# Kernel optimization log

Measured on AMD Instinct MI355X. Metric: run time of the kernel, lower is better.

The kernel has to match this reference:

```python
import jax, jax.numpy as jnp
import numpy as np

N, F, G, E, L, HID, C = 16384, 256, 64, 131072, 3, 512, 2
EPS = 1e-5
IU = F * (F - 1) // 2      # 32640 strict-upper-tri features per graph
IN1 = IU + F * L           # 33408 MLP input width


def setup_inputs() -> dict:
    key = jax.random.key(0)
    ks = jax.random.split(key, 16)

    def w(k, shape, fan_in):
        return jax.random.normal(k, shape, jnp.float32) * (1.0 / np.sqrt(fan_in))

    return {
        "x": jax.random.normal(ks[0], (N, F), jnp.float32),
        "edge_index": jax.random.randint(ks[1], (2, E), 0, N, dtype=jnp.int32),
        "batch": jnp.repeat(jnp.arange(G, dtype=jnp.int32), N // G),  # F nodes per graph
        "lin_src_w": w(ks[2], (L, F, F), F), "lin_src_b": jnp.zeros((L, F), jnp.float32),
        "lin_dst_w": w(ks[3], (L, F, F), F), "lin_dst_b": jnp.zeros((L, F), jnp.float32),
        "att_w": w(ks[4], (L, 2 * F, 1), 2 * F), "att_b": jnp.zeros((L, 1), jnp.float32),
        "bn_g": jnp.ones((IU,), jnp.float32), "bn_b": jnp.zeros((IU,), jnp.float32),
        "bnh_g": jnp.ones((F * L,), jnp.float32), "bnh_b": jnp.zeros((F * L,), jnp.float32),
        "w1": w(ks[5], (IN1, HID), IN1), "b1": jnp.zeros((HID,), jnp.float32),
        "g1": jnp.ones((HID,), jnp.float32), "be1": jnp.zeros((HID,), jnp.float32),
        "w2": w(ks[6], (HID, HID // 2), HID), "b2": jnp.zeros((HID // 2,), jnp.float32),
        "g2": jnp.ones((HID // 2,), jnp.float32), "be2": jnp.zeros((HID // 2,), jnp.float32),
        "w3": w(ks[7], (HID // 2, HID // 2), HID // 2), "b3": jnp.zeros((HID // 2,), jnp.float32),
        "g3": jnp.ones((HID // 2,), jnp.float32), "be3": jnp.zeros((HID // 2,), jnp.float32),
        "w4": w(ks[8], (HID // 2, C), HID // 2), "b4": jnp.zeros((C,), jnp.float32),
    }


def _bn(z, g, b):
    # BatchNorm1d (training-mode batch stats, biased variance, as torch uses for normalization)
    m = jnp.mean(z, 0)
    v = jnp.var(z, 0)
    return (z - m) * jax.lax.rsqrt(v + EPS) * g + b


def _conv(x, src, dst, Ws, bs, Wd, bd, Wa, ba):
    # EdgeLevelAttention layer (heads=1): gather -> concat -> linear -> softmax(heads) -> weighted scatter-add
    x_src = x @ Ws + bs                      # [N, F]
    x_dst = x @ Wd + bd                      # [N, F]
    x_j = x_src[src]                         # [E2, F] source features per edge
    x_i = x_dst[dst]                         # [E2, F] destination features per edge
    alpha = jax.nn.softmax(jnp.concatenate([x_i, x_j], -1) @ Wa + ba, axis=1)  # [E2, 1] (all ones for heads=1)
    msg = x_i * alpha                        # message uses x_i, as in the source
    return jax.ops.segment_sum(msg, dst, num_segments=N)


def reference(x, edge_index, batch, lin_src_w, lin_src_b, lin_dst_w, lin_dst_b,
              att_w, att_b, bn_g, bn_b, bnh_g, bnh_b,
              w1, b1, g1, be1, w2, b2, g2, be2, w3, b3, g3, be3, w4, b4):
    loops = jnp.arange(N, dtype=edge_index.dtype)          # add_self_loops
    src = jnp.concatenate([edge_index[0], loops])
    dst = jnp.concatenate([edge_index[1], loops])

    h = x
    pooled = []
    cnt = jax.ops.segment_sum(jnp.ones((N, 1), x.dtype), batch, num_segments=G)
    for l in range(L):
        h = _conv(h, src, dst, lin_src_w[l], lin_src_b[l],
                  lin_dst_w[l], lin_dst_b[l], att_w[l], att_b[l])
        pooled.append(jax.ops.segment_sum(h, batch, num_segments=G) / cnt)  # global_mean_pool

    iu = np.triu_indices(F, k=1)
    xt = x.reshape(G, F, F)[:, iu[0], iu[1]]               # strict upper triangle per graph [G, IU]
    xt = _bn(xt, bn_g, bn_b)
    hh = _bn(jnp.concatenate(pooled, 1), bnh_g, bnh_b)     # [G, F*L]
    z = jnp.concatenate([xt, hh], 1)                       # [G, IN1]

    z = jax.nn.relu(_bn(z @ w1 + b1, g1, be1))
    z = jax.nn.relu(_bn(z @ w2 + b2, g2, be2))
    z = jax.nn.relu(_bn(z @ w3 + b3, g3, be3))
    return z @ w4 + b4                                     # [G, C]
```

## Files before the change

### kernel.cpp

```cpp
#include <hip/hip_runtime.h>
#include <cstdint>

typedef __attribute__((ext_vector_type(8))) short short8;
typedef __attribute__((ext_vector_type(4))) float f32x4;
typedef unsigned short ushort_t;

static constexpr int NN = 16384, FF = 256, GG = 64, EE = 131072, LL = 3;
static constexpr int HIDN = 512, IU = 32640, IN1 = 33408;
#define EPSV 1e-5f

__device__ inline unsigned short bf16r(float v) {
  unsigned u = __float_as_uint(v);
  u += 0x7FFFu + ((u >> 16) & 1u);
  return (unsigned short)(u >> 16);
}

__global__ __launch_bounds__(256) void k_zero(int* __restrict__ p) {
  int i = blockIdx.x * 256 + threadIdx.x;
  if (i < 16448) p[i] = 0;
}

__global__ __launch_bounds__(256) void k_hist(const int* __restrict__ dst,
                                              const int* __restrict__ batch,
                                              int* __restrict__ deg, int* __restrict__ cnt) {
  __shared__ int hist[64];
  int bx = blockIdx.x, t = threadIdx.x;
  if (bx < 512) {
    int e = bx * 256 + t;
    atomicAdd(&deg[dst[e]], 1);
  } else {
    if (t < 64) hist[t] = 0;
    __syncthreads();
    int4 v = ((const int4*)batch)[(bx - 512) * 256 + t];
    int a[4] = {v.x, v.y, v.z, v.w};
    int cur = a[0], run = 1;
#pragma unroll
    for (int j = 1; j < 4; ++j) {
      if (a[j] == cur) run++;
      else { atomicAdd(&hist[cur], run); cur = a[j]; run = 1; }
    }
    atomicAdd(&hist[cur], run);
    __syncthreads();
    if (t < 64 && hist[t]) atomicAdd(&cnt[t], hist[t]);
  }
}

__global__ __launch_bounds__(256, 2) void k_conv(const float* __restrict__ A,
                                                 const float* __restrict__ W,
                                                 const float* __restrict__ bias,
                                                 const int* __restrict__ deg,
                                                 float* __restrict__ C,
                                                 float* __restrict__ pooled_p, int lofs) {
  __shared__ __align__(16) unsigned short Ah[64][72], Al[64][72];
  __shared__ __align__(16) unsigned short Bh[128][72], Bl[128][72];
  int n0 = blockIdx.x * 128, m0 = blockIdx.y * 64;
  int t = threadIdx.x;
  int w = t >> 6, l = t & 63;
  int wn = w * 32;
  int lr = l & 15, lg = l >> 4;
  f32x4 acc[4][2];
#pragma unroll
  for (int fm = 0; fm < 4; ++fm)
#pragma unroll
    for (int fn = 0; fn < 2; ++fn) acc[fm][fn] = (f32x4){0.f, 0.f, 0.f, 0.f};

  int am = t >> 2, aq = t & 3;
  int bkp = t & 3, bnf = (t >> 2) & 31, brr = t >> 7;

  for (int ks = 0; ks < 4; ++ks) {
    int k0 = ks * 64;
    if (ks) __syncthreads();
    {
      const float* ap = A + (size_t)(m0 + am) * FF + k0;
#pragma unroll
      for (int i = 0; i < 4; ++i) {
        int k = aq * 4 + i * 16;
        float4 v = *(const float4*)(ap + k);
        const float* vf = (const float*)&v;
        unsigned short h[4], lo[4];
#pragma unroll
        for (int j = 0; j < 4; ++j) {
          h[j] = bf16r(vf[j]);
          lo[j] = bf16r(vf[j] - __uint_as_float((unsigned)h[j] << 16));
        }
        *(uint2*)&Ah[am][k] = make_uint2((unsigned)h[0] | ((unsigned)h[1] << 16),
                                         (unsigned)h[2] | ((unsigned)h[3] << 16));
        *(uint2*)&Al[am][k] = make_uint2((unsigned)lo[0] | ((unsigned)lo[1] << 16),
                                         (unsigned)lo[2] | ((unsigned)lo[3] << 16));
      }
    }
#pragma unroll
    for (int r2 = 0; r2 < 4; ++r2) {
      int k = 2 * bkp + 8 * (brr * 4 + r2);
      const float* wp = W + (size_t)(k0 + k) * FF + n0 + bnf * 4;
      float4 va = *(const float4*)wp;
      float4 vb = *(const float4*)(wp + FF);
      const float* fa = (const float*)&va;
      const float* fb = (const float*)&vb;
#pragma unroll
      for (int j = 0; j < 4; ++j) {
        unsigned short ha = bf16r(fa[j]), hb = bf16r(fb[j]);
        unsigned short la = bf16r(fa[j] - __uint_as_float((unsigned)ha << 16));
        unsigned short lb = bf16r(fb[j] - __uint_as_float((unsigned)hb << 16));
        int n = bnf * 4 + j;
        *(unsigned*)&Bh[n][k] = (unsigned)ha | ((unsigned)hb << 16);
        *(unsigned*)&Bl[n][k] = (unsigned)la | ((unsigned)lb << 16);
      }
    }
    __syncthreads();
#pragma unroll
    for (int k2 = 0; k2 < 2; ++k2) {
      int kk = k2 * 32 + lg * 8;
      short8 afh[4], afl[4], bfh[2], bfl[2];
#pragma unroll
      for (int fm = 0; fm < 4; ++fm) {
        afh[fm] = *(const short8*)&Ah[fm * 16 + lr][kk];
        afl[fm] = *(const short8*)&Al[fm * 16 + lr][kk];
      }
#pragma unroll
      for (int fn = 0; fn < 2; ++fn) {
        bfh[fn] = *(const short8*)&Bh[wn + fn * 16 + lr][kk];
        bfl[fn] = *(const short8*)&Bl[wn + fn * 16 + lr][kk];
      }
#pragma unroll
      for (int fm = 0; fm < 4; ++fm)
#pragma unroll
        for (int fn = 0; fn < 2; ++fn) {
          acc[fm][fn] = __builtin_amdgcn_mfma_f32_16x16x32_bf16(afl[fm], bfh[fn], acc[fm][fn], 0, 0, 0);
          acc[fm][fn] = __builtin_amdgcn_mfma_f32_16x16x32_bf16(afh[fm], bfl[fn], acc[fm][fn], 0, 0, 0);
          acc[fm][fn] = __builtin_amdgcn_mfma_f32_16x16x32_bf16(afh[fm], bfh[fn], acc[fm][fn], 0, 0, 0);
        }
    }
  }
  float degf[4][4];
#pragma unroll
  for (int fm = 0; fm < 4; ++fm)
#pragma unroll
    for (int r = 0; r < 4; ++r)
      degf[fm][r] = (float)(deg[m0 + fm * 16 + lg * 4 + r] + 1);
  int g = blockIdx.y >> 2, sub = blockIdx.y & 3;
#pragma unroll
  for (int fn = 0; fn < 2; ++fn) {
    int col = n0 + wn + fn * 16 + lr;
    float bb = bias[col];
    float cs = 0.f;
#pragma unroll
    for (int fm = 0; fm < 4; ++fm) {
      const float* av = (const float*)&acc[fm][fn];
#pragma unroll
      for (int r = 0; r < 4; ++r) {
        int row = m0 + fm * 16 + lg * 4 + r;
        float v = (av[r] + bb) * degf[fm][r];
        if (C) C[(size_t)row * FF + col] = v;
        cs += v;
      }
    }
    cs += __shfl_xor(cs, 16);
    cs += __shfl_xor(cs, 32);
    if (lg == 0)
      pooled_p[((size_t)sub * 64 + g) * (FF * LL) + lofs + col] = cs;
  }
}

__global__ __launch_bounds__(1024, 1) void k_xt_bn(const float* __restrict__ x,
                                                   const float* __restrict__ bn_g,
                                                   const float* __restrict__ bn_b,
                                                   ushort_t* __restrict__ zh,
                                                   ushort_t* __restrict__ zl) {
  __shared__ float sb1[16][256], sb2[16][256];
  __shared__ float rsA[256], bbA[256];
  int i = blockIdx.x, t = threadIdx.x;
  int jq = t & 63, gq = t >> 6;
  int j4 = jq * 4;
  float4 vals[4];
  float s1[4] = {}, s2[4] = {};
#pragma unroll
  for (int r = 0; r < 4; ++r) {
    int g = gq * 4 + r;
    float4 vv = *(const float4*)(x + (size_t)(g * 256 + i) * FF + j4);
    vals[r] = vv;
    s1[0] += vv.x; s2[0] += vv.x * vv.x;
    s1[1] += vv.y; s2[1] += vv.y * vv.y;
    s1[2] += vv.z; s2[2] += vv.z * vv.z;
    s1[3] += vv.w; s2[3] += vv.w * vv.w;
  }
  *(float4*)&sb1[gq][j4] = make_float4(s1[0], s1[1], s1[2], s1[3]);
  *(float4*)&sb2[gq][j4] = make_float4(s2[0], s2[1], s2[2], s2[3]);
  __syncthreads();
  if (t < 256) {
    int j = t;
    float S1 = 0.f, S2 = 0.f;
#pragma unroll
    for (int q = 0; q < 16; ++q) { S1 += sb1[q][j]; S2 += sb2[q][j]; }
    float m = S1 * (1.f / 64.f);
    float var = S2 * (1.f / 64.f) - m * m;
    float rs = 0.f, bb = 0.f;
    if (j > i) {
      int p = i * 255 - (i * (i - 1)) / 2 + (j - i - 1);
      rs = rsqrtf(var + EPSV) * bn_g[p];
      bb = bn_b[p] - m * rs;
    }
    rsA[j] = rs;
    bbA[j] = bb;
  }
  __syncthreads();
  int P0 = i * 255 - (i * (i - 1)) / 2 - i - 1;
#pragma unroll
  for (int r = 0; r < 4; ++r) {
    int g = gq * 4 + r;
    size_t base = (size_t)g * IN1 + P0;
    const float* vf = (const float*)&vals[r];
#pragma unroll
    for (int jj = 0; jj < 4; ++jj) {
      int j = j4 + jj;
      if (j > i) {
        float f = vf[jj] * rsA[j] + bbA[j];
        unsigned short h = bf16r(f);
        zh[base + j] = h;
        zl[base + j] = bf16r(f - __uint_as_float((unsigned)h << 16));
      }
    }
  }
}

__global__ __launch_bounds__(256) void k_pool_bn(const float* __restrict__ pooled_p,
                                                 const int* __restrict__ cnt,
                                                 const float* __restrict__ bnh_g,
                                                 const float* __restrict__ bnh_b,
                                                 ushort_t* __restrict__ zh,
                                                 ushort_t* __restrict__ zl) {
  __shared__ float sb1[4][64], sb2[4][64], rsA[64], bbA[64];
  int bx = blockIdx.x, t = threadIdx.x;
  int ql = t & 63, gq = t >> 6;
  int q = bx * 64 + ql;
  float vals[16];
  float s1 = 0.f, s2 = 0.f;
#pragma unroll
  for (int gg = 0; gg < 16; ++gg) {
    int g = gq * 16 + gg;
    float v = (pooled_p[((size_t)0 * 64 + g) * (FF * LL) + q] +
               pooled_p[((size_t)1 * 64 + g) * (FF * LL) + q] +
               pooled_p[((size_t)2 * 64 + g) * (FF * LL) + q] +
               pooled_p[((size_t)3 * 64 + g) * (FF * LL) + q]) / (float)cnt[g];
    vals[gg] = v;
    s1 += v;
    s2 += v * v;
  }
  sb1[gq][ql] = s1;
  sb2[gq][ql] = s2;
  __syncthreads();
  if (t < 64) {
    float S1 = sb1[0][t] + sb1[1][t] + sb1[2][t] + sb1[3][t];
    float S2 = sb2[0][t] + sb2[1][t] + sb2[2][t] + sb2[3][t];
    float m = S1 * (1.f / 64.f);
    float var = S2 * (1.f / 64.f) - m * m;
    int qq = bx * 64 + t;
    float rs = rsqrtf(var + EPSV) * bnh_g[qq];
    rsA[t] = rs;
    bbA[t] = bnh_b[qq] - m * rs;
  }
  __syncthreads();
#pragma unroll
  for (int gg = 0; gg < 16; ++gg) {
    int g = gq * 16 + gg;
    float f = vals[gg] * rsA[ql] + bbA[ql];
    unsigned short h = bf16r(f);
    zh[(size_t)g * IN1 + IU + q] = h;
    zl[(size_t)g * IN1 + IU + q] = bf16r(f - __uint_as_float((unsigned)h << 16));
  }
}

__global__ __launch_bounds__(256, 4) void k_w1(const ushort_t* __restrict__ zh,
                                               const ushort_t* __restrict__ zl,
                                               const float* __restrict__ W,
                                               float* __restrict__ partial) {
  __shared__ __align__(16) unsigned short Zh[64][72], Zl[64][72];
  __shared__ __align__(16) unsigned short Wh[64][72], Wl[64][72];
  int nb = blockIdx.x, s = blockIdx.y;
  int t = threadIdx.x;
  int w = t >> 6, l = t & 63, lr = l & 15, lg = l >> 4;
  int ncol = nb * 64 + w * 16 + lr;
  f32x4 acc[4];
#pragma unroll
  for (int mt = 0; mt < 4; ++mt) acc[mt] = (f32x4){0.f, 0.f, 0.f, 0.f};

  for (int c = s; c < 522; c += 64) {
    int p0 = c * 64;
    if (c != s) __syncthreads();
#pragma unroll
    for (int it = 0; it < 2; ++it) {
      int idx = it * 256 + t;
      int g = idx >> 3, kq = idx & 7;
      *(uint4*)&Zh[g][kq * 8] = *(const uint4*)(zh + (size_t)g * IN1 + p0 + kq * 8);
      *(uint4*)&Zl[g][kq * 8] = *(const uint4*)(zl + (size_t)g * IN1 + p0 + kq * 8);
    }
#pragma unroll
    for (int it = 0; it < 2; ++it) {
      int idx = it * 256 + t;
      int kp = idx >> 4, cg = idx & 15;
      int k = kp * 2;
      const float* wp = W + (size_t)(p0 + k) * HIDN + nb * 64 + cg * 4;
      float4 va = *(const float4*)wp;
      float4 vb = *(const float4*)(wp + HIDN);
      const float* fa = (const float*)&va;
      const float* fb = (const float*)&vb;
#pragma unroll
      for (int j = 0; j < 4; ++j) {
        unsigned ua = __float_as_uint(fa[j]);
        unsigned ub = __float_as_uint(fb[j]);
        unsigned short ha = (unsigned short)(ua >> 16);
        unsigned short hb = (unsigned short)(ub >> 16);
        unsigned short la = bf16r(fa[j] - __uint_as_float(ua & 0xFFFF0000u));
        unsigned short lb = bf16r(fb[j] - __uint_as_float(ub & 0xFFFF0000u));
        int col = cg * 4 + j;
        *(unsigned*)&Wh[col][k] = (unsigned)ha | ((unsigned)hb << 16);
        *(unsigned*)&Wl[col][k] = (unsigned)la | ((unsigned)lb << 16);
      }
    }
    __syncthreads();
#pragma unroll
    for (int k2 = 0; k2 < 2; ++k2) {
      int kloc = k2 * 32 + lg * 8;
      short8 bh = *(const short8*)&Wh[w * 16 + lr][kloc];
      short8 bl = *(const short8*)&Wl[w * 16 + lr][kloc];
#pragma unroll
      for (int mt = 0; mt < 4; ++mt) {
        short8 ah = *(const short8*)&Zh[mt * 16 + lr][kloc];
        short8 al = *(const short8*)&Zl[mt * 16 + lr][kloc];
        acc[mt] = __builtin_amdgcn_mfma_f32_16x16x32_bf16(al, bh, acc[mt], 0, 0, 0);
        acc[mt] = __builtin_amdgcn_mfma_f32_16x16x32_bf16(ah, bl, acc[mt], 0, 0, 0);
        acc[mt] = __builtin_amdgcn_mfma_f32_16x16x32_bf16(ah, bh, acc[mt], 0, 0, 0);
      }
    }
  }
#pragma unroll
  for (int mt = 0; mt < 4; ++mt) {
    const float* av = (const float*)&acc[mt];
#pragma unroll
    for (int r = 0; r < 4; ++r) {
      int g = mt * 16 + lg * 4 + r;
      partial[((size_t)s * 64 + g) * HIDN + ncol] = av[r];
    }
  }
}

__global__ __launch_bounds__(256) void k_reduce(const float* __restrict__ partial,
                                                const float* __restrict__ bias,
                                                float* __restrict__ out, int S, int N) {
  int idx = blockIdx.x * 256 + threadIdx.x;
  if (idx >= 64 * N) return;
  int h = idx % N;
  float a = bias[h];
  for (int s = 0; s < S; ++s) a += partial[(size_t)s * 64 * N + idx];
  out[idx] = a;
}

__global__ __launch_bounds__(64) void k_bn_relu(const float* __restrict__ in,
                                                const float* __restrict__ gamma,
                                                const float* __restrict__ beta,
                                                float* __restrict__ out, int N) {
  int h = blockIdx.x;
  int g = threadIdx.x;
  float v = in[(size_t)g * N + h];
  float s = v, s2 = v * v;
#pragma unroll
  for (int o = 32; o > 0; o >>= 1) {
    s += __shfl_xor(s, o);
    s2 += __shfl_xor(s2, o);
  }
  float m = s * (1.f / 64.f);
  float var = s2 * (1.f / 64.f) - m * m;
  float r = (v - m) * rsqrtf(var + EPSV) * gamma[h] + beta[h];
  out[(size_t)g * N + h] = fmaxf(r, 0.f);
}

__global__ __launch_bounds__(256, 2) void k_mlp_small(const float* __restrict__ Z,
                                                      const float* __restrict__ W,
                                                      const float* __restrict__ bias,
                                                      const float* __restrict__ gamma,
                                                      const float* __restrict__ beta,
                                                      float* __restrict__ out, int K, int N) {
  __shared__ float Ws[512 * 16];
  __shared__ float zl[64][132];
  __shared__ float sb1[16][17], sb2[16][17];
  int t = threadIdx.x;
  int h0 = blockIdx.x * 16;
  for (int idx = t; idx < K * 4; idx += 256) {
    int r = idx >> 2, q = idx & 3;
    *(float4*)&Ws[r * 16 + q * 4] = *(const float4*)(W + (size_t)r * N + h0 + q * 4);
  }
  int c = t & 15, gq = t >> 4;
  float acc[4] = {};
  for (int ch = 0; ch < K; ch += 128) {
    for (int idx = t; idx < 64 * 32; idx += 256) {
      int g = idx >> 5, kq = idx & 31;
      *(float4*)&zl[g][kq * 4] = *(const float4*)(Z + (size_t)g * K + ch + kq * 4);
    }
    __syncthreads();
#pragma unroll 8
    for (int kk = 0; kk < 128; ++kk) {
      float w = Ws[(ch + kk) * 16 + c];
#pragma unroll
      for (int i = 0; i < 4; ++i) acc[i] = fmaf(zl[gq * 4 + i][kk], w, acc[i]);
    }
    __syncthreads();
  }
  float bb = bias[h0 + c];
  float s1 = 0.f, s2 = 0.f;
#pragma unroll
  for (int i = 0; i < 4; ++i) {
    acc[i] += bb;
    s1 += acc[i];
    s2 += acc[i] * acc[i];
  }
  sb1[gq][c] = s1;
  sb2[gq][c] = s2;
  __syncthreads();
  float S1 = 0.f, S2 = 0.f;
#pragma unroll
  for (int q = 0; q < 16; ++q) { S1 += sb1[q][c]; S2 += sb2[q][c]; }
  float m = S1 * (1.f / 64.f);
  float var = S2 * (1.f / 64.f) - m * m;
  float rs = rsqrtf(var + EPSV) * gamma[h0 + c];
  float be = beta[h0 + c];
#pragma unroll
  for (int i = 0; i < 4; ++i)
    out[(size_t)(gq * 4 + i) * N + h0 + c] = fmaxf((acc[i] - m) * rs + be, 0.f);
}

__global__ __launch_bounds__(256) void k_final(const float* __restrict__ A,
                                               const float* __restrict__ w4,
                                               const float* __restrict__ b4,
                                               float* __restrict__ out) {
  __shared__ float w4l[512];
  int t = threadIdx.x;
  w4l[t] = w4[t];
  w4l[256 + t] = w4[256 + t];
  __syncthreads();
  int w = t >> 6, l = t & 63;
  for (int g = w * 16; g < w * 16 + 16; ++g) {
    float4 av = *(const float4*)(A + (size_t)g * 256 + l * 4);
    float c0 = av.x * w4l[(l * 4 + 0) * 2] + av.y * w4l[(l * 4 + 1) * 2] +
               av.z * w4l[(l * 4 + 2) * 2] + av.w * w4l[(l * 4 + 3) * 2];
    float c1 = av.x * w4l[(l * 4 + 0) * 2 + 1] + av.y * w4l[(l * 4 + 1) * 2 + 1] +
               av.z * w4l[(l * 4 + 2) * 2 + 1] + av.w * w4l[(l * 4 + 3) * 2 + 1];
#pragma unroll
    for (int o = 32; o > 0; o >>= 1) {
      c0 += __shfl_xor(c0, o);
      c1 += __shfl_xor(c1, o);
    }
    if (l == 0) {
      out[g * 2 + 0] = c0 + b4[0];
      out[g * 2 + 1] = c1 + b4[1];
    }
  }
}

extern "C" void kernel_launch(void* const* d_in, const int* in_sizes, int n_in,
                              void* d_out, int out_size, void* d_ws, size_t ws_size,
                              hipStream_t stream) {
  const float* x = (const float*)d_in[0];
  const int* edge = (const int*)d_in[1];
  const int* batch = (const int*)d_in[2];
  const float* lin_dst_w = (const float*)d_in[5];
  const float* lin_dst_b = (const float*)d_in[6];
  const float* bn_g = (const float*)d_in[9];
  const float* bn_b = (const float*)d_in[10];
  const float* bnh_g = (const float*)d_in[11];
  const float* bnh_b = (const float*)d_in[12];
  const float* w1 = (const float*)d_in[13];
  const float* b1 = (const float*)d_in[14];
  const float* g1 = (const float*)d_in[15];
  const float* be1 = (const float*)d_in[16];
  const float* w2 = (const float*)d_in[17];
  const float* b2 = (const float*)d_in[18];
  const float* g2 = (const float*)d_in[19];
  const float* be2 = (const float*)d_in[20];
  const float* w3 = (const float*)d_in[21];
  const float* b3 = (const float*)d_in[22];
  const float* g3 = (const float*)d_in[23];
  const float* be3 = (const float*)d_in[24];
  const float* w4 = (const float*)d_in[25];
  const float* b4 = (const float*)d_in[26];
  const int* dstp = edge + EE;

  char* ws = (char*)d_ws;
  int* deg = (int*)(ws);
  int* cnt = (int*)(ws + 65536);
  float* bufA = (float*)(ws + 131072);
  float* bufB = (float*)(ws + 131072 + 16777216);
  float* pooled_p = (float*)(ws + 131072 + 2 * 16777216);
  char* tail = ws + 131072 + 2 * 16777216 + 786432;
  float* m1 = (float*)(tail);
  float* m1b = (float*)(tail + 131072);
  float* m2b = (float*)(tail + 262144);
  float* m3b = (float*)(tail + 262144 + 65536);
  ushort_t* zh = (ushort_t*)bufA;
  ushort_t* zlp = zh + (size_t)64 * IN1;
  float* partial = bufB;

  k_zero<<<65, 256, 0, stream>>>(deg);
  k_hist<<<528, 256, 0, stream>>>(dstp, batch, deg, cnt);

  k_conv<<<dim3(2, 256), 256, 0, stream>>>(x, lin_dst_w, lin_dst_b, deg, bufA, pooled_p, 0);
  k_conv<<<dim3(2, 256), 256, 0, stream>>>(bufA, lin_dst_w + (size_t)FF * FF,
                                           lin_dst_b + FF, deg, bufB, pooled_p, FF);
  k_conv<<<dim3(2, 256), 256, 0, stream>>>(bufB, lin_dst_w + (size_t)2 * FF * FF,
                                           lin_dst_b + 2 * FF, deg, (float*)nullptr,
                                           pooled_p, 2 * FF);

  k_xt_bn<<<256, 1024, 0, stream>>>(x, bn_g, bn_b, zh, zlp);
  k_pool_bn<<<12, 256, 0, stream>>>(pooled_p, cnt, bnh_g, bnh_b, zh, zlp);

  k_w1<<<dim3(8, 64), 256, 0, stream>>>(zh, zlp, w1, partial);
  k_reduce<<<128, 256, 0, stream>>>(partial, b1, m1, 64, HIDN);
  k_bn_relu<<<HIDN, 64, 0, stream>>>(m1, g1, be1, m1b, HIDN);

  k_mlp_small<<<16, 256, 0, stream>>>(m1b, w2, b2, g2, be2, m2b, HIDN, 256);
  k_mlp_small<<<16, 256, 0, stream>>>(m2b, w3, b3, g3, be3, m3b, 256, 256);

  k_final<<<1, 256, 0, stream>>>(m3b, w4, b4, (float*)d_out);
}
```

Before: 178.5 us.

## Fuse BN front kernels, fuse reduce+BN, widen w1 split-K, swap conv grid

Merges the upper-triangle BN kernel and the pooled BN kernel into one launch, and merges the split-K reduction with the BN+ReLU of the first MLP layer into one kernel. It also doubles the split-K count of the w1 GEMM (128 slices instead of 64) and swaps the conv grid so that consecutive blocks share the same weight column tile. The aim is fewer launches, more parallelism in the large w1 GEMM, and better L2 reuse in the conv. The cost is twice the partial-sum traffic, which the reduce kernel must read, and that reduce now runs on only 8 blocks.

```diff
diff --git a/kernel.cpp b/kernel.cpp
--- a/kernel.cpp
+++ b/kernel.cpp
@@ -53,7 +53,8 @@
                                                  float* __restrict__ pooled_p, int lofs) {
   __shared__ __align__(16) unsigned short Ah[64][72], Al[64][72];
   __shared__ __align__(16) unsigned short Bh[128][72], Bl[128][72];
-  int n0 = blockIdx.x * 128, m0 = blockIdx.y * 64;
+  int mb = blockIdx.x;
+  int n0 = blockIdx.y * 128, m0 = mb * 64;
   int t = threadIdx.x;
   int w = t >> 6, l = t & 63;
   int wn = w * 32;
@@ -138,7 +139,7 @@
 #pragma unroll
     for (int r = 0; r < 4; ++r)
       degf[fm][r] = (float)(deg[m0 + fm * 16 + lg * 4 + r] + 1);
-  int g = blockIdx.y >> 2, sub = blockIdx.y & 3;
+  int g = mb >> 2, sub = mb & 3;
 #pragma unroll
   for (int fn = 0; fn < 2; ++fn) {
     int col = n0 + wn + fn * 16 + lr;
@@ -162,111 +163,112 @@
   }
 }
 
-__global__ __launch_bounds__(1024, 1) void k_xt_bn(const float* __restrict__ x,
-                                                   const float* __restrict__ bn_g,
-                                                   const float* __restrict__ bn_b,
-                                                   ushort_t* __restrict__ zh,
-                                                   ushort_t* __restrict__ zl) {
-  __shared__ float sb1[16][256], sb2[16][256];
-  __shared__ float rsA[256], bbA[256];
-  int i = blockIdx.x, t = threadIdx.x;
-  int jq = t & 63, gq = t >> 6;
-  int j4 = jq * 4;
-  float4 vals[4];
-  float s1[4] = {}, s2[4] = {};
-#pragma unroll
-  for (int r = 0; r < 4; ++r) {
-    int g = gq * 4 + r;
-    float4 vv = *(const float4*)(x + (size_t)(g * 256 + i) * FF + j4);
-    vals[r] = vv;
-    s1[0] += vv.x; s2[0] += vv.x * vv.x;
-    s1[1] += vv.y; s2[1] += vv.y * vv.y;
-    s1[2] += vv.z; s2[2] += vv.z * vv.z;
-    s1[3] += vv.w; s2[3] += vv.w * vv.w;
-  }
-  *(float4*)&sb1[gq][j4] = make_float4(s1[0], s1[1], s1[2], s1[3]);
-  *(float4*)&sb2[gq][j4] = make_float4(s2[0], s2[1], s2[2], s2[3]);
-  __syncthreads();
-  if (t < 256) {
-    int j = t;
-    float S1 = 0.f, S2 = 0.f;
-#pragma unroll
-    for (int q = 0; q < 16; ++q) { S1 += sb1[q][j]; S2 += sb2[q][j]; }
-    float m = S1 * (1.f / 64.f);
-    float var = S2 * (1.f / 64.f) - m * m;
-    float rs = 0.f, bb = 0.f;
-    if (j > i) {
-      int p = i * 255 - (i * (i - 1)) / 2 + (j - i - 1);
-      rs = rsqrtf(var + EPSV) * bn_g[p];
-      bb = bn_b[p] - m * rs;
-    }
-    rsA[j] = rs;
-    bbA[j] = bb;
-  }
-  __syncthreads();
-  int P0 = i * 255 - (i * (i - 1)) / 2 - i - 1;
-#pragma unroll
-  for (int r = 0; r < 4; ++r) {
-    int g = gq * 4 + r;
-    size_t base = (size_t)g * IN1 + P0;
-    const float* vf = (const float*)&vals[r];
-#pragma unroll
-    for (int jj = 0; jj < 4; ++jj) {
-      int j = j4 + jj;
+__global__ __launch_bounds__(1024, 1) void k_bn_front(const float* __restrict__ x,
+                                                      const float* __restrict__ bn_g,
+                                                      const float* __restrict__ bn_b,
+                                                      const float* __restrict__ pooled_p,
+                                                      const int* __restrict__ cnt,
+                                                      const float* __restrict__ bnh_g,
+                                                      const float* __restrict__ bnh_b,
+                                                      ushort_t* __restrict__ zh,
+                                                      ushort_t* __restrict__ zl) {
+  if (blockIdx.x < 256) {
+    __shared__ float sb1[16][256], sb2[16][256];
+    __shared__ float rsA[256], bbA[256];
+    int i = blockIdx.x, t = threadIdx.x;
+    int jq = t & 63, gq = t >> 6;
+    int j4 = jq * 4;
+    float4 vals[4];
+    float s1[4] = {}, s2[4] = {};
+#pragma unroll
+    for (int r = 0; r < 4; ++r) {
+      int g = gq * 4 + r;
+      float4 vv = *(const float4*)(x + (size_t)(g * 256 + i) * FF + j4);
+      vals[r] = vv;
+      s1[0] += vv.x; s2[0] += vv.x * vv.x;
+      s1[1] += vv.y; s2[1] += vv.y * vv.y;
+      s1[2] += vv.z; s2[2] += vv.z * vv.z;
+      s1[3] += vv.w; s2[3] += vv.w * vv.w;
+    }
+    *(float4*)&sb1[gq][j4] = make_float4(s1[0], s1[1], s1[2], s1[3]);
+    *(float4*)&sb2[gq][j4] = make_float4(s2[0], s2[1], s2[2], s2[3]);
+    __syncthreads();
+    if (t < 256) {
+      int j = t;
+      float S1 = 0.f, S2 = 0.f;
+#pragma unroll
+      for (int q = 0; q < 16; ++q) { S1 += sb1[q][j]; S2 += sb2[q][j]; }
+      float m = S1 * (1.f / 64.f);
+      float var = S2 * (1.f / 64.f) - m * m;
+      float rs = 0.f, bb = 0.f;
       if (j > i) {
-        float f = vf[jj] * rsA[j] + bbA[j];
-        unsigned short h = bf16r(f);
-        zh[base + j] = h;
-        zl[base + j] = bf16r(f - __uint_as_float((unsigned)h << 16));
-      }
-    }
-  }
-}
-
-__global__ __launch_bounds__(256) void k_pool_bn(const float* __restrict__ pooled_p,
-                                                 const int* __restrict__ cnt,
-                                                 const float* __restrict__ bnh_g,
-                                                 const float* __restrict__ bnh_b,
-                                                 ushort_t* __restrict__ zh,
-                                                 ushort_t* __restrict__ zl) {
-  __shared__ float sb1[4][64], sb2[4][64], rsA[64], bbA[64];
-  int bx = blockIdx.x, t = threadIdx.x;
-  int ql = t & 63, gq = t >> 6;
-  int q = bx * 64 + ql;
-  float vals[16];
-  float s1 = 0.f, s2 = 0.f;
-#pragma unroll
-  for (int gg = 0; gg < 16; ++gg) {
-    int g = gq * 16 + gg;
-    float v = (pooled_p[((size_t)0 * 64 + g) * (FF * LL) + q] +
-               pooled_p[((size_t)1 * 64 + g) * (FF * LL) + q] +
-               pooled_p[((size_t)2 * 64 + g) * (FF * LL) + q] +
-               pooled_p[((size_t)3 * 64 + g) * (FF * LL) + q]) / (float)cnt[g];
-    vals[gg] = v;
-    s1 += v;
-    s2 += v * v;
-  }
-  sb1[gq][ql] = s1;
-  sb2[gq][ql] = s2;
-  __syncthreads();
-  if (t < 64) {
-    float S1 = sb1[0][t] + sb1[1][t] + sb1[2][t] + sb1[3][t];
-    float S2 = sb2[0][t] + sb2[1][t] + sb2[2][t] + sb2[3][t];
-    float m = S1 * (1.f / 64.f);
-    float var = S2 * (1.f / 64.f) - m * m;
-    int qq = bx * 64 + t;
-    float rs = rsqrtf(var + EPSV) * bnh_g[qq];
-    rsA[t] = rs;
-    bbA[t] = bnh_b[qq] - m * rs;
-  }
-  __syncthreads();
-#pragma unroll
-  for (int gg = 0; gg < 16; ++gg) {
-    int g = gq * 16 + gg;
-    float f = vals[gg] * rsA[ql] + bbA[ql];
-    unsigned short h = bf16r(f);
-    zh[(size_t)g * IN1 + IU + q] = h;
-    zl[(size_t)g * IN1 + IU + q] = bf16r(f - __uint_as_float((unsigned)h << 16));
+        int p = i * 255 - (i * (i - 1)) / 2 + (j - i - 1);
+        rs = rsqrtf(var + EPSV) * bn_g[p];
+        bb = bn_b[p] - m * rs;
+      }
+      rsA[j] = rs;
+      bbA[j] = bb;
+    }
+    __syncthreads();
+    int P0 = i * 255 - (i * (i - 1)) / 2 - i - 1;
+#pragma unroll
+    for (int r = 0; r < 4; ++r) {
+      int g = gq * 4 + r;
+      size_t base = (size_t)g * IN1 + P0;
+      const float* vf = (const float*)&vals[r];
+#pragma unroll
+      for (int jj = 0; jj < 4; ++jj) {
+        int j = j4 + jj;
+        if (j > i) {
+          float f = vf[jj] * rsA[j] + bbA[j];
+          unsigned short h = bf16r(f);
+          zh[base + j] = h;
+          zl[base + j] = bf16r(f - __uint_as_float((unsigned)h << 16));
+        }
+      }
+    }
+  } else {
+    __shared__ float pb1[4][64], pb2[4][64], prs[64], pbb[64];
+    int t = threadIdx.x;
+    if (t >= 256) return;
+    int bx = blockIdx.x - 256;
+    int ql = t & 63, gq = t >> 6;
+    int q = bx * 64 + ql;
+    float vals[16];
+    float s1 = 0.f, s2 = 0.f;
+#pragma unroll
+    for (int gg = 0; gg < 16; ++gg) {
+      int g = gq * 16 + gg;
+      float v = (pooled_p[((size_t)0 * 64 + g) * (FF * LL) + q] +
+                 pooled_p[((size_t)1 * 64 + g) * (FF * LL) + q] +
+                 pooled_p[((size_t)2 * 64 + g) * (FF * LL) + q] +
+                 pooled_p[((size_t)3 * 64 + g) * (FF * LL) + q]) / (float)cnt[g];
+      vals[gg] = v;
+      s1 += v;
+      s2 += v * v;
+    }
+    pb1[gq][ql] = s1;
+    pb2[gq][ql] = s2;
+    __syncthreads();
+    if (t < 64) {
+      float S1 = pb1[0][t] + pb1[1][t] + pb1[2][t] + pb1[3][t];
+      float S2 = pb2[0][t] + pb2[1][t] + pb2[2][t] + pb2[3][t];
+      float m = S1 * (1.f / 64.f);
+      float var = S2 * (1.f / 64.f) - m * m;
+      int qq = bx * 64 + t;
+      float rs = rsqrtf(var + EPSV) * bnh_g[qq];
+      prs[t] = rs;
+      pbb[t] = bnh_b[qq] - m * rs;
+    }
+    __syncthreads();
+#pragma unroll
+    for (int gg = 0; gg < 16; ++gg) {
+      int g = gq * 16 + gg;
+      float f = vals[gg] * prs[ql] + pbb[ql];
+      unsigned short h = bf16r(f);
+      zh[(size_t)g * IN1 + IU + q] = h;
+      zl[(size_t)g * IN1 + IU + q] = bf16r(f - __uint_as_float((unsigned)h << 16));
+    }
   }
 }
 
@@ -284,7 +286,7 @@
 #pragma unroll
   for (int mt = 0; mt < 4; ++mt) acc[mt] = (f32x4){0.f, 0.f, 0.f, 0.f};
 
-  for (int c = s; c < 522; c += 64) {
+  for (int c = s; c < 522; c += 128) {
     int p0 = c * 64;
     if (c != s) __syncthreads();
 #pragma unroll
@@ -344,34 +346,46 @@
   }
 }
 
-__global__ __launch_bounds__(256) void k_reduce(const float* __restrict__ partial,
-                                                const float* __restrict__ bias,
-                                                float* __restrict__ out, int S, int N) {
-  int idx = blockIdx.x * 256 + threadIdx.x;
-  if (idx >= 64 * N) return;
-  int h = idx % N;
-  float a = bias[h];
-  for (int s = 0; s < S; ++s) a += partial[(size_t)s * 64 * N + idx];
-  out[idx] = a;
-}
-
-__global__ __launch_bounds__(64) void k_bn_relu(const float* __restrict__ in,
-                                                const float* __restrict__ gamma,
-                                                const float* __restrict__ beta,
-                                                float* __restrict__ out, int N) {
-  int h = blockIdx.x;
-  int g = threadIdx.x;
-  float v = in[(size_t)g * N + h];
-  float s = v, s2 = v * v;
-#pragma unroll
-  for (int o = 32; o > 0; o >>= 1) {
-    s += __shfl_xor(s, o);
-    s2 += __shfl_xor(s2, o);
-  }
-  float m = s * (1.f / 64.f);
-  float var = s2 * (1.f / 64.f) - m * m;
-  float r = (v - m) * rsqrtf(var + EPSV) * gamma[h] + beta[h];
-  out[(size_t)g * N + h] = fmaxf(r, 0.f);
+__global__ __launch_bounds__(256) void k_rbn(const float* __restrict__ partial,
+                                             const float* __restrict__ bias,
+                                             const float* __restrict__ gamma,
+                                             const float* __restrict__ beta,
+                                             float* __restrict__ out, int S, int N) {
+  __shared__ float sb1[4][64], sb2[4][64], rsA[64], bbA[64];
+  int t = threadIdx.x;
+  int c = t & 63, gq = t >> 6;
+  int col = blockIdx.x * 64 + c;
+  float acc[16];
+  float bb = bias[col];
+  float s1 = 0.f, s2 = 0.f;
+#pragma unroll
+  for (int gg = 0; gg < 16; ++gg) {
+    int g = gq * 16 + gg;
+    float a = bb;
+    for (int s = 0; s < S; ++s) a += partial[((size_t)s * 64 + g) * N + col];
+    acc[gg] = a;
+    s1 += a;
+    s2 += a * a;
+  }
+  sb1[gq][c] = s1;
+  sb2[gq][c] = s2;
+  __syncthreads();
+  if (t < 64) {
+    float S1 = sb1[0][t] + sb1[1][t] + sb1[2][t] + sb1[3][t];
+    float S2 = sb2[0][t] + sb2[1][t] + sb2[2][t] + sb2[3][t];
+    float m = S1 * (1.f / 64.f);
+    float var = S2 * (1.f / 64.f) - m * m;
+    int cc = blockIdx.x * 64 + t;
+    float rs = rsqrtf(var + EPSV) * gamma[cc];
+    rsA[t] = rs;
+    bbA[t] = beta[cc] - m * rs;
+  }
+  __syncthreads();
+#pragma unroll
+  for (int gg = 0; gg < 16; ++gg) {
+    int g = gq * 16 + gg;
+    out[(size_t)g * N + col] = fmaxf(acc[gg] * rsA[c] + bbA[c], 0.f);
+  }
 }
 
 __global__ __launch_bounds__(256, 2) void k_mlp_small(const float* __restrict__ Z,
@@ -491,10 +505,9 @@
   float* bufB = (float*)(ws + 131072 + 16777216);
   float* pooled_p = (float*)(ws + 131072 + 2 * 16777216);
   char* tail = ws + 131072 + 2 * 16777216 + 786432;
-  float* m1 = (float*)(tail);
-  float* m1b = (float*)(tail + 131072);
-  float* m2b = (float*)(tail + 262144);
-  float* m3b = (float*)(tail + 262144 + 65536);
+  float* m1b = (float*)(tail);
+  float* m2b = (float*)(tail + 131072);
+  float* m3b = (float*)(tail + 131072 + 65536);
   ushort_t* zh = (ushort_t*)bufA;
   ushort_t* zlp = zh + (size_t)64 * IN1;
   float* partial = bufB;
@@ -502,19 +515,17 @@
   k_zero<<<65, 256, 0, stream>>>(deg);
   k_hist<<<528, 256, 0, stream>>>(dstp, batch, deg, cnt);
 
-  k_conv<<<dim3(2, 256), 256, 0, stream>>>(x, lin_dst_w, lin_dst_b, deg, bufA, pooled_p, 0);
-  k_conv<<<dim3(2, 256), 256, 0, stream>>>(bufA, lin_dst_w + (size_t)FF * FF,
+  k_conv<<<dim3(256, 2), 256, 0, stream>>>(x, lin_dst_w, lin_dst_b, deg, bufA, pooled_p, 0);
+  k_conv<<<dim3(256, 2), 256, 0, stream>>>(bufA, lin_dst_w + (size_t)FF * FF,
                                            lin_dst_b + FF, deg, bufB, pooled_p, FF);
-  k_conv<<<dim3(2, 256), 256, 0, stream>>>(bufB, lin_dst_w + (size_t)2 * FF * FF,
+  k_conv<<<dim3(256, 2), 256, 0, stream>>>(bufB, lin_dst_w + (size_t)2 * FF * FF,
                                            lin_dst_b + 2 * FF, deg, (float*)nullptr,
                                            pooled_p, 2 * FF);
 
-  k_xt_bn<<<256, 1024, 0, stream>>>(x, bn_g, bn_b, zh, zlp);
-  k_pool_bn<<<12, 256, 0, stream>>>(pooled_p, cnt, bnh_g, bnh_b, zh, zlp);
-
-  k_w1<<<dim3(8, 64), 256, 0, stream>>>(zh, zlp, w1, partial);
-  k_reduce<<<128, 256, 0, stream>>>(partial, b1, m1, 64, HIDN);
-  k_bn_relu<<<HIDN, 64, 0, stream>>>(m1, g1, be1, m1b, HIDN);
+  k_bn_front<<<268, 1024, 0, stream>>>(x, bn_g, bn_b, pooled_p, cnt, bnh_g, bnh_b, zh, zlp);
+
+  k_w1<<<dim3(8, 128), 256, 0, stream>>>(zh, zlp, w1, partial);
+  k_rbn<<<8, 256, 0, stream>>>(partial, b1, g1, be1, m1b, 128, HIDN);
 
   k_mlp_small<<<16, 256, 0, stream>>>(m1b, w2, b2, g2, be2, m2b, HIDN, 256);
   k_mlp_small<<<16, 256, 0, stream>>>(m2b, w3, b3, g3, be3, m3b, 256, 256);
```

Result: slower. 635.8 us (+256.1%).

## Swap conv grid order, fuse BN front kernels, double W1 split-K

Applied to the files above, without the earlier changes.

The conv GEMM grid is transposed so the row-block index becomes the fast blockIdx.x, which changes the order in which tiles are scheduled and how A and W are reused in cache. The two batch-norm preparation kernels are merged into one launch, with the pooled-feature branch running in extra blocks that use only 256 of their 1024 threads. The W1 split-K factor goes from 64 to 128 slices, adding parallelism but doubling the partial buffer that the reduce kernel has to read.

```diff
diff --git a/kernel.cpp b/kernel.cpp
--- a/kernel.cpp
+++ b/kernel.cpp
@@ -53,7 +53,8 @@
                                                  float* __restrict__ pooled_p, int lofs) {
   __shared__ __align__(16) unsigned short Ah[64][72], Al[64][72];
   __shared__ __align__(16) unsigned short Bh[128][72], Bl[128][72];
-  int n0 = blockIdx.x * 128, m0 = blockIdx.y * 64;
+  int mb = blockIdx.x;
+  int n0 = blockIdx.y * 128, m0 = mb * 64;
   int t = threadIdx.x;
   int w = t >> 6, l = t & 63;
   int wn = w * 32;
@@ -138,7 +139,7 @@
 #pragma unroll
     for (int r = 0; r < 4; ++r)
       degf[fm][r] = (float)(deg[m0 + fm * 16 + lg * 4 + r] + 1);
-  int g = blockIdx.y >> 2, sub = blockIdx.y & 3;
+  int g = mb >> 2, sub = mb & 3;
 #pragma unroll
   for (int fn = 0; fn < 2; ++fn) {
     int col = n0 + wn + fn * 16 + lr;
@@ -162,111 +163,112 @@
   }
 }
 
-__global__ __launch_bounds__(1024, 1) void k_xt_bn(const float* __restrict__ x,
-                                                   const float* __restrict__ bn_g,
-                                                   const float* __restrict__ bn_b,
-                                                   ushort_t* __restrict__ zh,
-                                                   ushort_t* __restrict__ zl) {
-  __shared__ float sb1[16][256], sb2[16][256];
-  __shared__ float rsA[256], bbA[256];
-  int i = blockIdx.x, t = threadIdx.x;
-  int jq = t & 63, gq = t >> 6;
-  int j4 = jq * 4;
-  float4 vals[4];
-  float s1[4] = {}, s2[4] = {};
-#pragma unroll
-  for (int r = 0; r < 4; ++r) {
-    int g = gq * 4 + r;
-    float4 vv = *(const float4*)(x + (size_t)(g * 256 + i) * FF + j4);
-    vals[r] = vv;
-    s1[0] += vv.x; s2[0] += vv.x * vv.x;
-    s1[1] += vv.y; s2[1] += vv.y * vv.y;
-    s1[2] += vv.z; s2[2] += vv.z * vv.z;
-    s1[3] += vv.w; s2[3] += vv.w * vv.w;
-  }
-  *(float4*)&sb1[gq][j4] = make_float4(s1[0], s1[1], s1[2], s1[3]);
-  *(float4*)&sb2[gq][j4] = make_float4(s2[0], s2[1], s2[2], s2[3]);
-  __syncthreads();
-  if (t < 256) {
-    int j = t;
-    float S1 = 0.f, S2 = 0.f;
-#pragma unroll
-    for (int q = 0; q < 16; ++q) { S1 += sb1[q][j]; S2 += sb2[q][j]; }
-    float m = S1 * (1.f / 64.f);
-    float var = S2 * (1.f / 64.f) - m * m;
-    float rs = 0.f, bb = 0.f;
-    if (j > i) {
-      int p = i * 255 - (i * (i - 1)) / 2 + (j - i - 1);
-      rs = rsqrtf(var + EPSV) * bn_g[p];
-      bb = bn_b[p] - m * rs;
-    }
-    rsA[j] = rs;
-    bbA[j] = bb;
-  }
-  __syncthreads();
-  int P0 = i * 255 - (i * (i - 1)) / 2 - i - 1;
-#pragma unroll
-  for (int r = 0; r < 4; ++r) {
-    int g = gq * 4 + r;
-    size_t base = (size_t)g * IN1 + P0;
-    const float* vf = (const float*)&vals[r];
-#pragma unroll
-    for (int jj = 0; jj < 4; ++jj) {
-      int j = j4 + jj;
+__global__ __launch_bounds__(1024, 1) void k_bn_front(const float* __restrict__ x,
+                                                      const float* __restrict__ bn_g,
+                                                      const float* __restrict__ bn_b,
+                                                      const float* __restrict__ pooled_p,
+                                                      const int* __restrict__ cnt,
+                                                      const float* __restrict__ bnh_g,
+                                                      const float* __restrict__ bnh_b,
+                                                      ushort_t* __restrict__ zh,
+                                                      ushort_t* __restrict__ zl) {
+  if (blockIdx.x < 256) {
+    __shared__ float sb1[16][256], sb2[16][256];
+    __shared__ float rsA[256], bbA[256];
+    int i = blockIdx.x, t = threadIdx.x;
+    int jq = t & 63, gq = t >> 6;
+    int j4 = jq * 4;
+    float4 vals[4];
+    float s1[4] = {}, s2[4] = {};
+#pragma unroll
+    for (int r = 0; r < 4; ++r) {
+      int g = gq * 4 + r;
+      float4 vv = *(const float4*)(x + (size_t)(g * 256 + i) * FF + j4);
+      vals[r] = vv;
+      s1[0] += vv.x; s2[0] += vv.x * vv.x;
+      s1[1] += vv.y; s2[1] += vv.y * vv.y;
+      s1[2] += vv.z; s2[2] += vv.z * vv.z;
+      s1[3] += vv.w; s2[3] += vv.w * vv.w;
+    }
+    *(float4*)&sb1[gq][j4] = make_float4(s1[0], s1[1], s1[2], s1[3]);
+    *(float4*)&sb2[gq][j4] = make_float4(s2[0], s2[1], s2[2], s2[3]);
+    __syncthreads();
+    if (t < 256) {
+      int j = t;
+      float S1 = 0.f, S2 = 0.f;
+#pragma unroll
+      for (int q = 0; q < 16; ++q) { S1 += sb1[q][j]; S2 += sb2[q][j]; }
+      float m = S1 * (1.f / 64.f);
+      float var = S2 * (1.f / 64.f) - m * m;
+      float rs = 0.f, bb = 0.f;
       if (j > i) {
-        float f = vf[jj] * rsA[j] + bbA[j];
-        unsigned short h = bf16r(f);
-        zh[base + j] = h;
-        zl[base + j] = bf16r(f - __uint_as_float((unsigned)h << 16));
-      }
-    }
-  }
-}
-
-__global__ __launch_bounds__(256) void k_pool_bn(const float* __restrict__ pooled_p,
-                                                 const int* __restrict__ cnt,
-                                                 const float* __restrict__ bnh_g,
-                                                 const float* __restrict__ bnh_b,
-                                                 ushort_t* __restrict__ zh,
-                                                 ushort_t* __restrict__ zl) {
-  __shared__ float sb1[4][64], sb2[4][64], rsA[64], bbA[64];
-  int bx = blockIdx.x, t = threadIdx.x;
-  int ql = t & 63, gq = t >> 6;
-  int q = bx * 64 + ql;
-  float vals[16];
-  float s1 = 0.f, s2 = 0.f;
-#pragma unroll
-  for (int gg = 0; gg < 16; ++gg) {
-    int g = gq * 16 + gg;
-    float v = (pooled_p[((size_t)0 * 64 + g) * (FF * LL) + q] +
-               pooled_p[((size_t)1 * 64 + g) * (FF * LL) + q] +
-               pooled_p[((size_t)2 * 64 + g) * (FF * LL) + q] +
-               pooled_p[((size_t)3 * 64 + g) * (FF * LL) + q]) / (float)cnt[g];
-    vals[gg] = v;
-    s1 += v;
-    s2 += v * v;
-  }
-  sb1[gq][ql] = s1;
-  sb2[gq][ql] = s2;
-  __syncthreads();
-  if (t < 64) {
-    float S1 = sb1[0][t] + sb1[1][t] + sb1[2][t] + sb1[3][t];
-    float S2 = sb2[0][t] + sb2[1][t] + sb2[2][t] + sb2[3][t];
-    float m = S1 * (1.f / 64.f);
-    float var = S2 * (1.f / 64.f) - m * m;
-    int qq = bx * 64 + t;
-    float rs = rsqrtf(var + EPSV) * bnh_g[qq];
-    rsA[t] = rs;
-    bbA[t] = bnh_b[qq] - m * rs;
-  }
-  __syncthreads();
-#pragma unroll
-  for (int gg = 0; gg < 16; ++gg) {
-    int g = gq * 16 + gg;
-    float f = vals[gg] * rsA[ql] + bbA[ql];
-    unsigned short h = bf16r(f);
-    zh[(size_t)g * IN1 + IU + q] = h;
-    zl[(size_t)g * IN1 + IU + q] = bf16r(f - __uint_as_float((unsigned)h << 16));
+        int p = i * 255 - (i * (i - 1)) / 2 + (j - i - 1);
+        rs = rsqrtf(var + EPSV) * bn_g[p];
+        bb = bn_b[p] - m * rs;
+      }
+      rsA[j] = rs;
+      bbA[j] = bb;
+    }
+    __syncthreads();
+    int P0 = i * 255 - (i * (i - 1)) / 2 - i - 1;
+#pragma unroll
+    for (int r = 0; r < 4; ++r) {
+      int g = gq * 4 + r;
+      size_t base = (size_t)g * IN1 + P0;
+      const float* vf = (const float*)&vals[r];
+#pragma unroll
+      for (int jj = 0; jj < 4; ++jj) {
+        int j = j4 + jj;
+        if (j > i) {
+          float f = vf[jj] * rsA[j] + bbA[j];
+          unsigned short h = bf16r(f);
+          zh[base + j] = h;
+          zl[base + j] = bf16r(f - __uint_as_float((unsigned)h << 16));
+        }
+      }
+    }
+  } else {
+    __shared__ float pb1[4][64], pb2[4][64], prs[64], pbb[64];
+    int t = threadIdx.x;
+    if (t >= 256) return;
+    int bx = blockIdx.x - 256;
+    int ql = t & 63, gq = t >> 6;
+    int q = bx * 64 + ql;
+    float vals[16];
+    float s1 = 0.f, s2 = 0.f;
+#pragma unroll
+    for (int gg = 0; gg < 16; ++gg) {
+      int g = gq * 16 + gg;
+      float v = (pooled_p[((size_t)0 * 64 + g) * (FF * LL) + q] +
+                 pooled_p[((size_t)1 * 64 + g) * (FF * LL) + q] +
+                 pooled_p[((size_t)2 * 64 + g) * (FF * LL) + q] +
+                 pooled_p[((size_t)3 * 64 + g) * (FF * LL) + q]) / (float)cnt[g];
+      vals[gg] = v;
+      s1 += v;
+      s2 += v * v;
+    }
+    pb1[gq][ql] = s1;
+    pb2[gq][ql] = s2;
+    __syncthreads();
+    if (t < 64) {
+      float S1 = pb1[0][t] + pb1[1][t] + pb1[2][t] + pb1[3][t];
+      float S2 = pb2[0][t] + pb2[1][t] + pb2[2][t] + pb2[3][t];
+      float m = S1 * (1.f / 64.f);
+      float var = S2 * (1.f / 64.f) - m * m;
+      int qq = bx * 64 + t;
+      float rs = rsqrtf(var + EPSV) * bnh_g[qq];
+      prs[t] = rs;
+      pbb[t] = bnh_b[qq] - m * rs;
+    }
+    __syncthreads();
+#pragma unroll
+    for (int gg = 0; gg < 16; ++gg) {
+      int g = gq * 16 + gg;
+      float f = vals[gg] * prs[ql] + pbb[ql];
+      unsigned short h = bf16r(f);
+      zh[(size_t)g * IN1 + IU + q] = h;
+      zl[(size_t)g * IN1 + IU + q] = bf16r(f - __uint_as_float((unsigned)h << 16));
+    }
   }
 }
 
@@ -284,7 +286,7 @@
 #pragma unroll
   for (int mt = 0; mt < 4; ++mt) acc[mt] = (f32x4){0.f, 0.f, 0.f, 0.f};
 
-  for (int c = s; c < 522; c += 64) {
+  for (int c = s; c < 522; c += 128) {
     int p0 = c * 64;
     if (c != s) __syncthreads();
 #pragma unroll
@@ -502,18 +504,17 @@
   k_zero<<<65, 256, 0, stream>>>(deg);
   k_hist<<<528, 256, 0, stream>>>(dstp, batch, deg, cnt);
 
-  k_conv<<<dim3(2, 256), 256, 0, stream>>>(x, lin_dst_w, lin_dst_b, deg, bufA, pooled_p, 0);
-  k_conv<<<dim3(2, 256), 256, 0, stream>>>(bufA, lin_dst_w + (size_t)FF * FF,
+  k_conv<<<dim3(256, 2), 256, 0, stream>>>(x, lin_dst_w, lin_dst_b, deg, bufA, pooled_p, 0);
+  k_conv<<<dim3(256, 2), 256, 0, stream>>>(bufA, lin_dst_w + (size_t)FF * FF,
                                            lin_dst_b + FF, deg, bufB, pooled_p, FF);
-  k_conv<<<dim3(2, 256), 256, 0, stream>>>(bufB, lin_dst_w + (size_t)2 * FF * FF,
+  k_conv<<<dim3(256, 2), 256, 0, stream>>>(bufB, lin_dst_w + (size_t)2 * FF * FF,
                                            lin_dst_b + 2 * FF, deg, (float*)nullptr,
                                            pooled_p, 2 * FF);
 
-  k_xt_bn<<<256, 1024, 0, stream>>>(x, bn_g, bn_b, zh, zlp);
-  k_pool_bn<<<12, 256, 0, stream>>>(pooled_p, cnt, bnh_g, bnh_b, zh, zlp);
-
-  k_w1<<<dim3(8, 64), 256, 0, stream>>>(zh, zlp, w1, partial);
-  k_reduce<<<128, 256, 0, stream>>>(partial, b1, m1, 64, HIDN);
+  k_bn_front<<<268, 1024, 0, stream>>>(x, bn_g, bn_b, pooled_p, cnt, bnh_g, bnh_b, zh, zlp);
+
+  k_w1<<<dim3(8, 128), 256, 0, stream>>>(zh, zlp, w1, partial);
+  k_reduce<<<128, 256, 0, stream>>>(partial, b1, m1, 128, HIDN);
   k_bn_relu<<<HIDN, 64, 0, stream>>>(m1, g1, be1, m1b, HIDN);
 
   k_mlp_small<<<16, 256, 0, stream>>>(m1b, w2, b2, g2, be2, m2b, HIDN, 256);
```

New measurement: 187.3 us. +4.9%, slower.
